# Kernel optimization log

Hardware: AMD Instinct MI355X
Metric: run time of the kernel (lower is better)

The kernel has to match this reference:

```python
import jax, jax.numpy as jnp
import numpy as np


def setup_inputs() -> dict:
    key = jax.random.key(0)
    k1, k2, k3 = jax.random.split(key, 3)
    B, C, H, W = 32, 2048, 14, 14
    OUT = 512
    x = jax.random.normal(k1, (B, C, H, W), dtype=jnp.float32)
    gamma = jnp.zeros((1,), dtype=jnp.float32)  # nn.Parameter(torch.zeros(1))
    # 1x1 conv 2048 -> 512 (layer=4 branch), kaiming-ish scale
    conv_w = jax.random.normal(k2, (OUT, C, 1, 1), dtype=jnp.float32) * (1.0 / np.sqrt(C))
    conv_b = jax.random.normal(k3, (OUT,), dtype=jnp.float32) * 0.01
    return {"x": x, "gamma": gamma, "conv_w": conv_w, "conv_b": conv_b}


def reference(x, gamma, conv_w, conv_b):
    B, C, H, W = x.shape
    q = x.reshape(B, C, H * W)                      # [B, C, N]
    # energy[b, c, d] = <q[b,c,:], q[b,d,:]>
    energy = jnp.einsum('bcn,bdn->bcd', q, q)       # [B, C, C]
    # max-subtract trick: softmax(max - energy) along last dim
    energy_new = jnp.max(energy, axis=-1, keepdims=True) - energy
    attention = jax.nn.softmax(energy_new, axis=-1)  # [B, C, C]
    out = jnp.einsum('bcd,bdn->bcn', attention, q).reshape(B, C, H, W)
    out = gamma * out + x
    # 1x1 conv, stride 1, no padding (layer=4 branch)
    pam_out = jax.lax.conv_general_dilated(
        out, conv_w, window_strides=(1, 1), padding='VALID',
        dimension_numbers=('NCHW', 'OIHW', 'NCHW'))
    pam_out = pam_out + conv_b[None, :, None, None]
    return pam_out
```

## Files before the change

kernel.cpp:

```cpp
#include <hip/hip_runtime.h>
#include <stdint.h>

#define B_   32
#define C_   2048
#define HW_  196
#define OUT_ 512
#define KT_  64
#define BPITCH 66

typedef short short8 __attribute__((ext_vector_type(8)));
typedef float floatx4 __attribute__((ext_vector_type(4)));
typedef unsigned short u16;

__device__ __forceinline__ u16 f2bf(float f) {
  union { float f; uint32_t u; } v; v.f = f;
  return (u16)((v.u + 0x8000u) >> 16);
}

__global__ void wcvt_kernel(const float* __restrict__ w, u16* __restrict__ wbf) {
  int gid = blockIdx.x * 256 + threadIdx.x;
  float4 v = ((const float4*)w)[gid];
  uint32_t lo = (uint32_t)f2bf(v.x) | ((uint32_t)f2bf(v.y) << 16);
  uint32_t hi = (uint32_t)f2bf(v.z) | ((uint32_t)f2bf(v.w) << 16);
  ((uint2*)wbf)[gid] = make_uint2(lo, hi);
}

__global__ void attn_fallback(const float* __restrict__ x, const float* __restrict__ gamma,
                              float* __restrict__ y) {
  float g = gamma[0];
  if (g == 0.0f) return;
  __shared__ float qc[HW_];
  __shared__ float e[C_];
  __shared__ float red[256];
  int tid = threadIdx.x;
  for (int cRow = blockIdx.x; cRow < C_; cRow += gridDim.x) {
    for (int b = 0; b < B_; ++b) {
      const float* q = x + (size_t)b * C_ * HW_;
      __syncthreads();
      for (int i = tid; i < HW_; i += 256) qc[i] = q[(size_t)cRow * HW_ + i];
      __syncthreads();
      for (int d = tid; d < C_; d += 256) {
        float s = 0.f;
        const float* qd = q + (size_t)d * HW_;
        for (int n = 0; n < HW_; ++n) s += qc[n] * qd[n];
        e[d] = s;
      }
      __syncthreads();
      float mn = 3.4e38f;
      for (int d = tid; d < C_; d += 256) mn = fminf(mn, e[d]);
      red[tid] = mn; __syncthreads();
      for (int s = 128; s > 0; s >>= 1) { if (tid < s) red[tid] = fminf(red[tid], red[tid + s]); __syncthreads(); }
      float emin = red[0];
      __syncthreads();
      float ps = 0.f;
      for (int d = tid; d < C_; d += 256) { float p = __expf(emin - e[d]); e[d] = p; ps += p; }
      red[tid] = ps; __syncthreads();
      for (int s = 128; s > 0; s >>= 1) { if (tid < s) red[tid] += red[tid + s]; __syncthreads(); }
      float S = red[0];
      __syncthreads();
      float invS = 1.f / S;
      for (int n = tid; n < HW_; n += 256) {
        float acc = 0.f;
        for (int d = 0; d < C_; ++d) acc += e[d] * q[(size_t)d * HW_ + n];
        y[((size_t)b * C_ + cRow) * HW_ + n] = g * acc * invS + q[(size_t)cRow * HW_ + n];
      }
    }
  }
}

__global__ __launch_bounds__(256, 1) void conv_gemm(
    const float* __restrict__ x, const float* __restrict__ yws,
    const u16* __restrict__ wbf, const float* __restrict__ bias,
    const float* __restrict__ gamma, float* __restrict__ out) {

  __shared__ __align__(16) u16 As[128 * 64];
  __shared__ __align__(16) u16 Bs[112 * BPITCH];

  const float* src = (gamma[0] != 0.f) ? yws : x;

  int bid  = blockIdx.x;
  int b    = bid >> 3;
  int mIdx = (bid >> 1) & 3;
  int nIdx = bid & 1;
  int oBase = mIdx * 128;
  int n0    = nIdx * 112;

  int tid  = threadIdx.x;
  int wave = tid >> 6;
  int lane = tid & 63;
  int col  = lane & 15;
  int quad = lane >> 4;

  const float* xb = src + (size_t)b * C_ * HW_;

  floatx4 acc[2][7];
#pragma unroll
  for (int i = 0; i < 2; ++i)
#pragma unroll
    for (int j = 0; j < 7; ++j) { floatx4 z = {0.f, 0.f, 0.f, 0.f}; acc[i][j] = z; }

  int aO[4], aCb[4];
#pragma unroll
  for (int j = 0; j < 4; ++j) {
    int s = j * 256 + tid;
    aO[j]  = s >> 3;
    aCb[j] = (s & 7) ^ (aO[j] & 7);
  }
  int bN4[7], bC[7];
  bool bValid[7];
#pragma unroll
  for (int i = 0; i < 7; ++i) {
    int tau = i * 256 + tid;
    bN4[i] = tau % 28;
    bC[i]  = tau / 28;
    bValid[i] = (n0 + bN4[i] * 4) < HW_;
  }

  uint4  aReg[4];
  float4 bReg[7];

  auto loadTile = [&](int kBase) {
#pragma unroll
    for (int j = 0; j < 4; ++j)
      aReg[j] = *(const uint4*)(wbf + (size_t)(oBase + aO[j]) * C_ + kBase + aCb[j] * 8);
#pragma unroll
    for (int i = 0; i < 7; ++i) {
      if (bValid[i])
        bReg[i] = *(const float4*)(xb + (size_t)(kBase + bC[i]) * HW_ + n0 + bN4[i] * 4);
      else
        bReg[i] = make_float4(0.f, 0.f, 0.f, 0.f);
    }
  };

  loadTile(0);

  for (int kt = 0; kt < C_ / KT_; ++kt) {
    __syncthreads();
#pragma unroll
    for (int j = 0; j < 4; ++j)
      ((uint4*)As)[j * 256 + tid] = aReg[j];
#pragma unroll
    for (int i = 0; i < 7; ++i) {
      int nl = bN4[i] * 4;
      int c  = bC[i];
      Bs[(nl + 0) * BPITCH + c] = f2bf(bReg[i].x);
      Bs[(nl + 1) * BPITCH + c] = f2bf(bReg[i].y);
      Bs[(nl + 2) * BPITCH + c] = f2bf(bReg[i].z);
      Bs[(nl + 3) * BPITCH + c] = f2bf(bReg[i].w);
    }
    if (kt + 1 < C_ / KT_) loadTile((kt + 1) * KT_);
    __syncthreads();

    const short8* as8  = (const short8*)As;
    const uint32_t* bs32 = (const uint32_t*)Bs;
#pragma unroll
    for (int ks = 0; ks < 2; ++ks) {
      short8 af[2];
#pragma unroll
      for (int mt = 0; mt < 2; ++mt) {
        int o  = wave * 32 + mt * 16 + col;
        int cb = ks * 4 + quad;
        af[mt] = as8[o * 8 + (cb ^ (o & 7))];
      }
#pragma unroll
      for (int nt = 0; nt < 7; ++nt) {
        int n = nt * 16 + col;
        int base = (n * BPITCH + ks * 32 + quad * 8) >> 1;
        union { uint32_t u[4]; short8 v; } bb;
        bb.u[0] = bs32[base + 0];
        bb.u[1] = bs32[base + 1];
        bb.u[2] = bs32[base + 2];
        bb.u[3] = bs32[base + 3];
#pragma unroll
        for (int mt = 0; mt < 2; ++mt)
          acc[mt][nt] = __builtin_amdgcn_mfma_f32_16x16x32_bf16(af[mt], bb.v, acc[mt][nt], 0, 0, 0);
      }
    }
  }

  float* outb = out + (size_t)b * OUT_ * HW_;
#pragma unroll
  for (int mt = 0; mt < 2; ++mt) {
#pragma unroll
    for (int nt = 0; nt < 7; ++nt) {
      int n = n0 + nt * 16 + col;
      if (n < HW_) {
#pragma unroll
        for (int r = 0; r < 4; ++r) {
          int o = oBase + wave * 32 + mt * 16 + quad * 4 + r;
          outb[(size_t)o * HW_ + n] = acc[mt][nt][r] + bias[o];
        }
      }
    }
  }
}

extern "C" void kernel_launch(void* const* d_in, const int* in_sizes, int n_in,
                              void* d_out, int out_size, void* d_ws, size_t ws_size,
                              hipStream_t stream) {
  const float* x      = (const float*)d_in[0];
  const float* gamma  = (const float*)d_in[1];
  const float* conv_w = (const float*)d_in[2];
  const float* conv_b = (const float*)d_in[3];
  float* out = (float*)d_out;

  const size_t wbf_bytes = (size_t)OUT_ * C_ * sizeof(u16);
  const size_t y_bytes   = (size_t)B_ * C_ * HW_ * sizeof(float);
  u16*   wbf = (u16*)d_ws;
  float* yws = (float*)((char*)d_ws + wbf_bytes);
  bool have_fallback_ws = ws_size >= wbf_bytes + y_bytes;
  const float* ysrc = have_fallback_ws ? (const float*)yws : x;

  wcvt_kernel<<<dim3((OUT_ * C_) / 4 / 256), dim3(256), 0, stream>>>(conv_w, wbf);
  if (have_fallback_ws)
    attn_fallback<<<dim3(256), dim3(256), 0, stream>>>(x, gamma, yws);
  conv_gemm<<<dim3(256), dim3(256), 0, stream>>>(x, ysrc, wbf, conv_b, gamma, out);
}
```

Before: 151.4 us.

## Shrink conv GEMM N-tile to 28 and launch XCD-aware grid of 896 blocks

The 1x1-conv GEMM tile shrinks from 128x112 to 128x28 output columns, which raises the grid from 256 to 896 blocks. Launch bounds are raised so several blocks can share a CU, and the block-to-tile mapping groups tiles by XCD for better L2 locality on the activations. The aim is more latency hiding and parallelism for a kernel that was running one low-occupancy block per CU. The cost is that each block now reloads the full bf16 weight slice for fewer columns, raising weight traffic, and each wave has less MFMA work per K step.

```diff
diff --git a/kernel.cpp b/kernel.cpp
--- a/kernel.cpp
+++ b/kernel.cpp
@@ -6,6 +6,8 @@
 #define HW_  196
 #define OUT_ 512
 #define KT_  64
+#define MT_  128
+#define NT_  28
 #define BPITCH 66
 
 typedef short short8 __attribute__((ext_vector_type(8)));
@@ -68,22 +70,25 @@
   }
 }
 
-__global__ __launch_bounds__(256, 1) void conv_gemm(
+__global__ __launch_bounds__(256, 4) void conv_gemm(
     const float* __restrict__ x, const float* __restrict__ yws,
     const u16* __restrict__ wbf, const float* __restrict__ bias,
     const float* __restrict__ gamma, float* __restrict__ out) {
 
-  __shared__ __align__(16) u16 As[128 * 64];
-  __shared__ __align__(16) u16 Bs[112 * BPITCH];
+  __shared__ __align__(16) u16 As[MT_ * KT_];
+  __shared__ __align__(16) u16 Bs[32 * BPITCH];
 
   const float* src = (gamma[0] != 0.f) ? yws : x;
 
-  int bid  = blockIdx.x;
-  int b    = bid >> 3;
-  int mIdx = (bid >> 1) & 3;
-  int nIdx = bid & 1;
-  int oBase = mIdx * 128;
-  int n0    = nIdx * 112;
+  int xcd  = blockIdx.x & 7;
+  int slot = blockIdx.x >> 3;
+  int mIdx = slot / 28;
+  int gIdx = slot % 28;
+  int g    = xcd + 8 * gIdx;
+  int b    = g / 7;
+  int nIdx = g % 7;
+  int oBase = mIdx * MT_;
+  int n0    = nIdx * NT_;
 
   int tid  = threadIdx.x;
   int wave = tid >> 6;
@@ -93,11 +98,11 @@
 
   const float* xb = src + (size_t)b * C_ * HW_;
 
-  floatx4 acc[2][7];
+  floatx4 acc[2][2];
 #pragma unroll
   for (int i = 0; i < 2; ++i)
 #pragma unroll
-    for (int j = 0; j < 7; ++j) { floatx4 z = {0.f, 0.f, 0.f, 0.f}; acc[i][j] = z; }
+    for (int j = 0; j < 2; ++j) { floatx4 z = {0.f, 0.f, 0.f, 0.f}; acc[i][j] = z; }
 
   int aO[4], aCb[4];
 #pragma unroll
@@ -106,30 +111,27 @@
     aO[j]  = s >> 3;
     aCb[j] = (s & 7) ^ (aO[j] & 7);
   }
-  int bN4[7], bC[7];
-  bool bValid[7];
-#pragma unroll
-  for (int i = 0; i < 7; ++i) {
+  int bN4[2], bC[2];
+  bool bValid[2];
+#pragma unroll
+  for (int i = 0; i < 2; ++i) {
     int tau = i * 256 + tid;
-    bN4[i] = tau % 28;
-    bC[i]  = tau / 28;
-    bValid[i] = (n0 + bN4[i] * 4) < HW_;
+    bN4[i] = tau % 7;
+    bC[i]  = tau / 7;
+    bValid[i] = bC[i] < KT_;
   }
 
   uint4  aReg[4];
-  float4 bReg[7];
+  float4 bReg[2];
 
   auto loadTile = [&](int kBase) {
 #pragma unroll
     for (int j = 0; j < 4; ++j)
       aReg[j] = *(const uint4*)(wbf + (size_t)(oBase + aO[j]) * C_ + kBase + aCb[j] * 8);
 #pragma unroll
-    for (int i = 0; i < 7; ++i) {
+    for (int i = 0; i < 2; ++i)
       if (bValid[i])
         bReg[i] = *(const float4*)(xb + (size_t)(kBase + bC[i]) * HW_ + n0 + bN4[i] * 4);
-      else
-        bReg[i] = make_float4(0.f, 0.f, 0.f, 0.f);
-    }
   };
 
   loadTile(0);
@@ -140,18 +142,20 @@
     for (int j = 0; j < 4; ++j)
       ((uint4*)As)[j * 256 + tid] = aReg[j];
 #pragma unroll
-    for (int i = 0; i < 7; ++i) {
-      int nl = bN4[i] * 4;
-      int c  = bC[i];
-      Bs[(nl + 0) * BPITCH + c] = f2bf(bReg[i].x);
-      Bs[(nl + 1) * BPITCH + c] = f2bf(bReg[i].y);
-      Bs[(nl + 2) * BPITCH + c] = f2bf(bReg[i].z);
-      Bs[(nl + 3) * BPITCH + c] = f2bf(bReg[i].w);
+    for (int i = 0; i < 2; ++i) {
+      if (bValid[i]) {
+        int nl = bN4[i] * 4;
+        int c  = bC[i];
+        Bs[(nl + 0) * BPITCH + c] = f2bf(bReg[i].x);
+        Bs[(nl + 1) * BPITCH + c] = f2bf(bReg[i].y);
+        Bs[(nl + 2) * BPITCH + c] = f2bf(bReg[i].z);
+        Bs[(nl + 3) * BPITCH + c] = f2bf(bReg[i].w);
+      }
     }
     if (kt + 1 < C_ / KT_) loadTile((kt + 1) * KT_);
     __syncthreads();
 
-    const short8* as8  = (const short8*)As;
+    const short8* as8    = (const short8*)As;
     const uint32_t* bs32 = (const uint32_t*)Bs;
 #pragma unroll
     for (int ks = 0; ks < 2; ++ks) {
@@ -163,7 +167,7 @@
         af[mt] = as8[o * 8 + (cb ^ (o & 7))];
       }
 #pragma unroll
-      for (int nt = 0; nt < 7; ++nt) {
+      for (int nt = 0; nt < 2; ++nt) {
         int n = nt * 16 + col;
         int base = (n * BPITCH + ks * 32 + quad * 8) >> 1;
         union { uint32_t u[4]; short8 v; } bb;
@@ -182,9 +186,10 @@
 #pragma unroll
   for (int mt = 0; mt < 2; ++mt) {
 #pragma unroll
-    for (int nt = 0; nt < 7; ++nt) {
-      int n = n0 + nt * 16 + col;
-      if (n < HW_) {
+    for (int nt = 0; nt < 2; ++nt) {
+      int nl = nt * 16 + col;
+      if (nl < NT_) {
+        int n = n0 + nl;
 #pragma unroll
         for (int r = 0; r < 4; ++r) {
           int o = oBase + wave * 32 + mt * 16 + quad * 4 + r;
@@ -214,5 +219,5 @@
   wcvt_kernel<<<dim3((OUT_ * C_) / 4 / 256), dim3(256), 0, stream>>>(conv_w, wbf);
   if (have_fallback_ws)
     attn_fallback<<<dim3(256), dim3(256), 0, stream>>>(x, gamma, yws);
-  conv_gemm<<<dim3(256), dim3(256), 0, stream>>>(x, ysrc, wbf, conv_b, gamma, out);
-}
+  conv_gemm<<<dim3(896), dim3(256), 0, stream>>>(x, ysrc, wbf, conv_b, gamma, out);
+}
```

New measurement: 265.1 us. +75.1%, slower.

## Shrink GEMM M-tile, load weights straight to registers, XCD-aware block mapping

Applied to the files above, without the earlier changes.

The conv GEMM output-channel tile shrinks from 128 to 64 and the grid doubles to 512 blocks, with launch bounds raised to two blocks per CU. The weight fragments now go straight from global memory into registers, so the A shared-memory buffer and its swizzle are gone. Activations are loaded four channels at a time and stored to LDS as packed bf16 pairs with a 136-element pitch, and block ids are remapped so each XCD shares the same batch/column slices for L2 reuse. The aim is higher occupancy, less LDS traffic and better cache locality, at the cost of each block reusing its B tile across fewer output channels and using scalar strided global loads for x.

```diff
diff --git a/kernel.cpp b/kernel.cpp
--- a/kernel.cpp
+++ b/kernel.cpp
@@ -1,4 +1,5 @@
 #include <hip/hip_runtime.h>
+#include <hip/hip_bf16.h>
 #include <stdint.h>
 
 #define B_   32
@@ -6,7 +7,8 @@
 #define HW_  196
 #define OUT_ 512
 #define KT_  64
-#define BPITCH 66
+#define MT_  64
+#define BP16 136
 
 typedef short short8 __attribute__((ext_vector_type(8)));
 typedef float floatx4 __attribute__((ext_vector_type(4)));
@@ -17,12 +19,16 @@
   return (u16)((v.u + 0x8000u) >> 16);
 }
 
+__device__ __forceinline__ uint32_t pack_bf16(float a, float b) {
+  union { __hip_bfloat162 h; uint32_t u; } c;
+  c.h = __float22bfloat162_rn(make_float2(a, b));
+  return c.u;
+}
+
 __global__ void wcvt_kernel(const float* __restrict__ w, u16* __restrict__ wbf) {
   int gid = blockIdx.x * 256 + threadIdx.x;
   float4 v = ((const float4*)w)[gid];
-  uint32_t lo = (uint32_t)f2bf(v.x) | ((uint32_t)f2bf(v.y) << 16);
-  uint32_t hi = (uint32_t)f2bf(v.z) | ((uint32_t)f2bf(v.w) << 16);
-  ((uint2*)wbf)[gid] = make_uint2(lo, hi);
+  ((uint2*)wbf)[gid] = make_uint2(pack_bf16(v.x, v.y), pack_bf16(v.z, v.w));
 }
 
 __global__ void attn_fallback(const float* __restrict__ x, const float* __restrict__ gamma,
@@ -68,22 +74,26 @@
   }
 }
 
-__global__ __launch_bounds__(256, 1) void conv_gemm(
+__global__ __launch_bounds__(256, 2) void conv_gemm(
     const float* __restrict__ x, const float* __restrict__ yws,
     const u16* __restrict__ wbf, const float* __restrict__ bias,
     const float* __restrict__ gamma, float* __restrict__ out) {
 
-  __shared__ __align__(16) u16 As[128 * 64];
-  __shared__ __align__(16) u16 Bs[112 * BPITCH];
+  __shared__ __align__(16) u16 Bs[112 * BP16];
 
   const float* src = (gamma[0] != 0.f) ? yws : x;
 
-  int bid  = blockIdx.x;
-  int b    = bid >> 3;
-  int mIdx = (bid >> 1) & 3;
-  int nIdx = bid & 1;
-  int oBase = mIdx * 128;
-  int n0    = nIdx * 112;
+  int bid = blockIdx.x;
+  int xcd = bid & 7;
+  int s   = bid >> 3;
+  int ot  = s & 7;
+  int g   = ((s >> 3) << 3) | xcd;
+  int b   = g >> 1;
+  int nh  = g & 1;
+  int oBase = ot * MT_;
+  int n0    = nh * 112;
+  int nLim  = HW_ - n0;
+  if (nLim > 112) nLim = 112;
 
   int tid  = threadIdx.x;
   int wave = tid >> 6;
@@ -92,105 +102,82 @@
   int quad = lane >> 4;
 
   const float* xb = src + (size_t)b * C_ * HW_;
-
-  floatx4 acc[2][7];
-#pragma unroll
-  for (int i = 0; i < 2; ++i)
-#pragma unroll
-    for (int j = 0; j < 7; ++j) { floatx4 z = {0.f, 0.f, 0.f, 0.f}; acc[i][j] = z; }
-
-  int aO[4], aCb[4];
-#pragma unroll
-  for (int j = 0; j < 4; ++j) {
-    int s = j * 256 + tid;
-    aO[j]  = s >> 3;
-    aCb[j] = (s & 7) ^ (aO[j] & 7);
-  }
-  int bN4[7], bC[7];
-  bool bValid[7];
+  int oWave = oBase + wave * 16 + col;
+
+  floatx4 acc[7];
+#pragma unroll
+  for (int i = 0; i < 7; ++i) { floatx4 z = {0.f, 0.f, 0.f, 0.f}; acc[i] = z; }
+
+  int sN[7], sCq[7]; bool sV[7];
 #pragma unroll
   for (int i = 0; i < 7; ++i) {
-    int tau = i * 256 + tid;
-    bN4[i] = tau % 28;
-    bC[i]  = tau / 28;
-    bValid[i] = (n0 + bN4[i] * 4) < HW_;
-  }
-
-  uint4  aReg[4];
+    int slot = i * 256 + tid;
+    sN[i]  = slot % 112;
+    sCq[i] = slot / 112;
+    sV[i]  = (n0 + sN[i]) < HW_;
+  }
+
   float4 bReg[7];
-
-  auto loadTile = [&](int kBase) {
-#pragma unroll
-    for (int j = 0; j < 4; ++j)
-      aReg[j] = *(const uint4*)(wbf + (size_t)(oBase + aO[j]) * C_ + kBase + aCb[j] * 8);
+  uint4  aReg[2], aRegN[2];
+
+  auto loadB = [&](int kBase) {
 #pragma unroll
     for (int i = 0; i < 7; ++i) {
-      if (bValid[i])
-        bReg[i] = *(const float4*)(xb + (size_t)(kBase + bC[i]) * HW_ + n0 + bN4[i] * 4);
-      else
-        bReg[i] = make_float4(0.f, 0.f, 0.f, 0.f);
+      if (sV[i]) {
+        const float* p = xb + (size_t)(kBase + sCq[i] * 4) * HW_ + n0 + sN[i];
+        bReg[i].x = p[0];
+        bReg[i].y = p[HW_];
+        bReg[i].z = p[2 * HW_];
+        bReg[i].w = p[3 * HW_];
+      }
     }
   };
-
-  loadTile(0);
+  auto loadA = [&](uint4* dst, int kBase) {
+#pragma unroll
+    for (int ks = 0; ks < 2; ++ks)
+      dst[ks] = *(const uint4*)(wbf + (size_t)oWave * C_ + kBase + ks * 32 + quad * 8);
+  };
+
+  loadB(0);
+  loadA(aReg, 0);
 
   for (int kt = 0; kt < C_ / KT_; ++kt) {
     __syncthreads();
 #pragma unroll
-    for (int j = 0; j < 4; ++j)
-      ((uint4*)As)[j * 256 + tid] = aReg[j];
-#pragma unroll
     for (int i = 0; i < 7; ++i) {
-      int nl = bN4[i] * 4;
-      int c  = bC[i];
-      Bs[(nl + 0) * BPITCH + c] = f2bf(bReg[i].x);
-      Bs[(nl + 1) * BPITCH + c] = f2bf(bReg[i].y);
-      Bs[(nl + 2) * BPITCH + c] = f2bf(bReg[i].z);
-      Bs[(nl + 3) * BPITCH + c] = f2bf(bReg[i].w);
-    }
-    if (kt + 1 < C_ / KT_) loadTile((kt + 1) * KT_);
+      uint32_t d0 = pack_bf16(bReg[i].x, bReg[i].y);
+      uint32_t d1 = pack_bf16(bReg[i].z, bReg[i].w);
+      *(uint2*)&Bs[sN[i] * BP16 + sCq[i] * 4] = make_uint2(d0, d1);
+    }
     __syncthreads();
 
-    const short8* as8  = (const short8*)As;
-    const uint32_t* bs32 = (const uint32_t*)Bs;
+    if (kt + 1 < C_ / KT_) {
+      loadB((kt + 1) * KT_);
+      loadA(aRegN, (kt + 1) * KT_);
+    }
+
 #pragma unroll
     for (int ks = 0; ks < 2; ++ks) {
-      short8 af[2];
-#pragma unroll
-      for (int mt = 0; mt < 2; ++mt) {
-        int o  = wave * 32 + mt * 16 + col;
-        int cb = ks * 4 + quad;
-        af[mt] = as8[o * 8 + (cb ^ (o & 7))];
-      }
+      union { uint4 u; short8 v; } af; af.u = aReg[ks];
 #pragma unroll
       for (int nt = 0; nt < 7; ++nt) {
-        int n = nt * 16 + col;
-        int base = (n * BPITCH + ks * 32 + quad * 8) >> 1;
-        union { uint32_t u[4]; short8 v; } bb;
-        bb.u[0] = bs32[base + 0];
-        bb.u[1] = bs32[base + 1];
-        bb.u[2] = bs32[base + 2];
-        bb.u[3] = bs32[base + 3];
-#pragma unroll
-        for (int mt = 0; mt < 2; ++mt)
-          acc[mt][nt] = __builtin_amdgcn_mfma_f32_16x16x32_bf16(af[mt], bb.v, acc[mt][nt], 0, 0, 0);
-      }
-    }
+        short8 bf = *(const short8*)&Bs[(nt * 16 + col) * BP16 + ks * 32 + quad * 8];
+        acc[nt] = __builtin_amdgcn_mfma_f32_16x16x32_bf16(af.v, bf, acc[nt], 0, 0, 0);
+      }
+    }
+    aReg[0] = aRegN[0]; aReg[1] = aRegN[1];
   }
 
   float* outb = out + (size_t)b * OUT_ * HW_;
 #pragma unroll
-  for (int mt = 0; mt < 2; ++mt) {
+  for (int r = 0; r < 4; ++r) {
+    int o = oBase + wave * 16 + quad * 4 + r;
+    float bv = bias[o];
+    float* orow = outb + (size_t)o * HW_ + n0;
 #pragma unroll
     for (int nt = 0; nt < 7; ++nt) {
-      int n = n0 + nt * 16 + col;
-      if (n < HW_) {
-#pragma unroll
-        for (int r = 0; r < 4; ++r) {
-          int o = oBase + wave * 32 + mt * 16 + quad * 4 + r;
-          outb[(size_t)o * HW_ + n] = acc[mt][nt][r] + bias[o];
-        }
-      }
+      int nl = nt * 16 + col;
+      if (nl < nLim) orow[nl] = acc[nt][r] + bv;
     }
   }
 }
@@ -214,5 +201,5 @@
   wcvt_kernel<<<dim3((OUT_ * C_) / 4 / 256), dim3(256), 0, stream>>>(conv_w, wbf);
   if (have_fallback_ws)
     attn_fallback<<<dim3(256), dim3(256), 0, stream>>>(x, gamma, yws);
-  conv_gemm<<<dim3(256), dim3(256), 0, stream>>>(x, ysrc, wbf, conv_b, gamma, out);
-}
+  conv_gemm<<<dim3(512), dim3(256), 0, stream>>>(x, ysrc, wbf, conv_b, gamma, out);
+}
```

New measurement: 144.7 us. 4.4% less time.
